# Kernel optimization log

Hardware: AMD Instinct MI355X
Metric: run time of the kernel (lower is better)

## Reference

```python
import jax, jax.numpy as jnp
import numpy as np

OBS_DIM = 512
BACKBONE_DIMS = [1024, 1024, 512]
EXPERT_HIDDEN = 256
NUM_EXPERTS = 16
NUM_ACTIONS = 32
BATCH = 65536


def _glorot(key, shape):
    fan_in = shape[-2] if len(shape) >= 2 else shape[-1]
    return jax.random.normal(key, shape, dtype=jnp.float32) * (1.0 / np.sqrt(fan_in))


def setup_inputs() -> dict:
    key = jax.random.key(0)
    ks = jax.random.split(key, 16)
    inp = {}
    inp['obs'] = jax.random.normal(ks[0], (BATCH, OBS_DIM), dtype=jnp.float32)
    # shared backbone: 512->1024->1024->512 (Linear+ReLU+Dropout(eval=identity))
    dims = [OBS_DIM] + BACKBONE_DIMS
    for i in range(3):
        inp[f'Wb{i}'] = _glorot(ks[1 + i], (dims[i], dims[i + 1]))
        inp[f'bb{i}'] = jnp.zeros((dims[i + 1],), dtype=jnp.float32)
    # experts, batched over expert dim: 512->256->ReLU->256->32
    inp['We1'] = _glorot(ks[4], (NUM_EXPERTS, BACKBONE_DIMS[-1], EXPERT_HIDDEN))
    inp['be1'] = jnp.zeros((NUM_EXPERTS, EXPERT_HIDDEN), dtype=jnp.float32)
    inp['We2'] = _glorot(ks[5], (NUM_EXPERTS, EXPERT_HIDDEN, NUM_ACTIONS))
    inp['be2'] = jnp.zeros((NUM_EXPERTS, NUM_ACTIONS), dtype=jnp.float32)
    # motion selector: 512->256->128->16 + softmax
    inp['Ws0'] = _glorot(ks[6], (OBS_DIM, 256))
    inp['bs0'] = jnp.zeros((256,), dtype=jnp.float32)
    inp['Ws1'] = _glorot(ks[7], (256, 128))
    inp['bs1'] = jnp.zeros((128,), dtype=jnp.float32)
    inp['Ws2'] = _glorot(ks[8], (128, NUM_EXPERTS))
    inp['bs2'] = jnp.zeros((NUM_EXPERTS,), dtype=jnp.float32)
    return inp


def reference(obs, Wb0, bb0, Wb1, bb1, Wb2, bb2, We1, be1, We2, be2,
              Ws0, bs0, Ws1, bs1, Ws2, bs2):
    # shared backbone (Dropout is identity in eval/inference)
    h = jax.nn.relu(obs @ Wb0 + bb0)
    h = jax.nn.relu(h @ Wb1 + bb1)
    h = jax.nn.relu(h @ Wb2 + bb2)  # [B, 512]
    # all experts on shared features, as one batched GEMM
    eh = jax.nn.relu(jnp.einsum('bd,edh->beh', h, We1) + be1)       # [B, E, 256]
    expert_actions = jnp.einsum('beh,eha->bea', eh, We2) + be2       # [B, E, A]
    # motion selector (softmax fusion weights)
    s = jax.nn.relu(obs @ Ws0 + bs0)
    s = jax.nn.relu(s @ Ws1 + bs1)
    w = jax.nn.softmax(s @ Ws2 + bs2, axis=-1)                        # [B, E]
    # softmax-weighted fusion over experts
    fused = jnp.einsum('bea,be->ba', expert_actions, w)              # [B, A]
    return fused
```

## Files before the change

kernel.cpp:

```cpp
#include <hip/hip_runtime.h>
#include <hip/hip_bf16.h>
#include <stdint.h>

typedef __attribute__((ext_vector_type(8))) short short8;
typedef __attribute__((ext_vector_type(4))) float f32x4;

__device__ __forceinline__ float b2f(short s) {
    union { unsigned u; float f; } v; v.u = ((unsigned)(unsigned short)s) << 16; return v.f;
}
__device__ __forceinline__ short f2b(float f) {
    union { float f; unsigned u; } v; v.f = f;
    unsigned r = (v.u + 0x7FFF + ((v.u >> 16) & 1)) >> 16;
    return (short)r;
}

__device__ __forceinline__ void gload16(const void* g, void* l) {
    __builtin_amdgcn_global_load_lds(
        (const __attribute__((address_space(1))) void*)(uintptr_t)g,
        (__attribute__((address_space(3))) void*)(uintptr_t)l,
        16, 0, 0);
}

#define BAR()    asm volatile("s_barrier" ::: "memory")
#define WAITV0() asm volatile("s_waitcnt vmcnt(0)" ::: "memory")
#define WAITL0() asm volatile("s_waitcnt lgkmcnt(0)" ::: "memory")
#define SGB()    __builtin_amdgcn_sched_barrier(0)

__global__ __launch_bounds__(256) void cast_bf16_kernel(
    const float* __restrict__ src, short* __restrict__ dst, int n8) {
    int i = blockIdx.x * 256 + threadIdx.x;
    if (i >= n8) return;
    const float4* s = (const float4*)src + (size_t)i * 2;
    float4 x0 = s[0], x1 = s[1];
    short8 o;
    o[0] = f2b(x0.x); o[1] = f2b(x0.y); o[2] = f2b(x0.z); o[3] = f2b(x0.w);
    o[4] = f2b(x1.x); o[5] = f2b(x1.y); o[6] = f2b(x1.z); o[7] = f2b(x1.w);
    *((short8*)dst + i) = o;
}

__global__ __launch_bounds__(256) void transpose_cast_kernel(
    const float* __restrict__ W, short* __restrict__ Wt, int K, int N, int total) {
    int t = blockIdx.x * 256 + threadIdx.x;
    if (t >= total) return;
    const float* src = W + (size_t)blockIdx.y * K * N;
    short* dst = Wt + (size_t)blockIdx.y * K * N;
    int n = t % N;
    int k0 = (t / N) * 8;
    short8 o;
#pragma unroll
    for (int i = 0; i < 8; i++) o[i] = f2b(src[(size_t)(k0 + i) * N + n]);
    *(short8*)(dst + (size_t)n * K + k0) = o;
}

__global__ __launch_bounds__(256, 3)
void gemm_bt_bias_relu(const short* __restrict__ A, const short* __restrict__ Bt,
                       const float* __restrict__ bias, short* __restrict__ C,
                       int M, int N, int K) {
    __shared__ __align__(16) short As[128 * 32];
    __shared__ __align__(16) short Bs[128 * 32];
    const int tid = threadIdx.x;
    const int w = tid >> 6, lane = tid & 63;
    const int tm = blockIdx.y * 128, tn = blockIdx.x * 128;
    const int wm = (w & 1) * 64, wn = (w >> 1) * 64;
    const int r = lane & 15, q = lane >> 4, qk = q * 8;

    const int c0 = w * 2, c1 = w * 2 + 1;
    const int srow0 = c0 * 16 + (lane >> 2);
    const int srow1 = c1 * 16 + (lane >> 2);
    const int skk = (lane & 3) * 8;
    const short* gA0 = A + (size_t)(tm + srow0) * K + skk;
    const short* gA1 = A + (size_t)(tm + srow1) * K + skk;
    const short* gB0 = Bt + (size_t)(tn + srow0) * K + skk;
    const short* gB1 = Bt + (size_t)(tn + srow1) * K + skk;
    short* lA0 = &As[c0 * 512]; short* lA1 = &As[c1 * 512];
    short* lB0 = &Bs[c0 * 512]; short* lB1 = &Bs[c1 * 512];

    f32x4 acc[4][4] = {};
    for (int k0 = 0; k0 < K; k0 += 32) {
        gload16(gA0 + k0, lA0);
        gload16(gA1 + k0, lA1);
        gload16(gB0 + k0, lB0);
        gload16(gB1 + k0, lB1);
        __syncthreads();
        short8 a[4], b[4];
#pragma unroll
        for (int i = 0; i < 4; i++) a[i] = *(const short8*)&As[(wm + i * 16 + r) * 32 + qk];
#pragma unroll
        for (int j = 0; j < 4; j++) b[j] = *(const short8*)&Bs[(wn + j * 16 + r) * 32 + qk];
#pragma unroll
        for (int i = 0; i < 4; i++)
#pragma unroll
            for (int j = 0; j < 4; j++)
                acc[i][j] = __builtin_amdgcn_mfma_f32_16x16x32_bf16(a[i], b[j], acc[i][j], 0, 0, 0);
        __syncthreads();
    }
#pragma unroll
    for (int j = 0; j < 4; j++) {
        int col = tn + wn + j * 16 + r;
        float bj = bias[col];
#pragma unroll
        for (int i = 0; i < 4; i++)
#pragma unroll
            for (int rr = 0; rr < 4; rr++) {
                int row = tm + wm + i * 16 + q * 4 + rr;
                float v = fmaxf(acc[i][j][rr] + bj, 0.f);
                C[(size_t)row * N + col] = f2b(v);
            }
    }
}

__global__ __launch_bounds__(256)
void selector_softmax(const short* __restrict__ s1, const short* __restrict__ Ws2t,
                      const float* __restrict__ bs2, float* __restrict__ wsel) {
    int tid = threadIdx.x;
    int row = blockIdx.x * 16 + (tid >> 4);
    int e = tid & 15;
    const short8* a = (const short8*)(s1 + (size_t)row * 128);
    const short8* b = (const short8*)(Ws2t + (size_t)e * 128);
    float acc = bs2[e];
#pragma unroll
    for (int kk = 0; kk < 16; ++kk) {
        short8 av = a[kk], bv = b[kk];
#pragma unroll
        for (int i = 0; i < 8; i++) acc = fmaf(b2f(av[i]), b2f(bv[i]), acc);
    }
    float m = acc;
#pragma unroll
    for (int off = 8; off >= 1; off >>= 1) m = fmaxf(m, __shfl_xor(m, off, 16));
    float ex = __expf(acc - m);
    float s = ex;
#pragma unroll
    for (int off = 8; off >= 1; off >>= 1) s += __shfl_xor(s, off, 16);
    wsel[(size_t)row * 16 + e] = ex / s;
}

__global__ __launch_bounds__(256)
void out_init_kernel(const float* __restrict__ wsel, const float* __restrict__ be2,
                     float* __restrict__ out) {
    int i = blockIdx.x * 256 + threadIdx.x;
    int row = i >> 5, a = i & 31;
    const float* wr = wsel + (size_t)row * 16;
    float acc = 0.f;
#pragma unroll
    for (int e = 0; e < 16; e++) acc = fmaf(wr[e], be2[e * 32 + a], acc);
    out[i] = acc;
}

__global__ __launch_bounds__(256)
void reduce_kernel(const float* __restrict__ partial, float* __restrict__ out) {
    int t = blockIdx.x * 256 + threadIdx.x;
    int a4 = t & 7, i = t >> 3;
    int by = i >> 8, r = i & 255;
    const float* p = partial + (size_t)by * 16 * 8192 + r * 32 + a4 * 4;
    f32x4 s = *(const f32x4*)(out + (size_t)i * 32 + a4 * 4);
#pragma unroll
    for (int bx = 0; bx < 16; bx++) s += *(const f32x4*)(p + (size_t)bx * 8192);
    *(f32x4*)(out + (size_t)i * 32 + a4 * 4) = s;
}

template<int MODE>
__global__ __launch_bounds__(512, 2)
void gemm256(const short* __restrict__ A, const short* __restrict__ Bt,
             const float* __restrict__ bias, const float* __restrict__ wselp,
             const short* __restrict__ W2, short* __restrict__ C,
             float* __restrict__ pout, int M, int N, int K) {
    extern __shared__ __align__(16) short lds[];
    const int tid = threadIdx.x;
    const int w = tid >> 6, lane = tid & 63;
    const int wr = w >> 2, wc = w & 3;

    const int gx = gridDim.x;
    const int b = blockIdx.y * gx + blockIdx.x;
    const int per = (gx * gridDim.y) >> 3;
    const int sb = (b & 7) * per + (b >> 3);
    const int bx = sb % gx, by = sb / gx;
    const int tm = by * 256, tn = bx * 256;

    const int rih = w * 8 + (lane >> 3);
    const int colel = (((lane & 7) ^ (lane >> 3)) << 3);
    const short* pA = A + (size_t)(tm + rih) * K + colel;
    const short* pB = Bt + (size_t)(tn + rih) * K + colel;
    const size_t rK64 = (size_t)64 * K, rK128 = (size_t)128 * K;
    short* const ldsw = lds + w * 512;

#define STG_A(buf, h, t) do { \
        const short* s_ = pA + (size_t)(h) * rK128 + (size_t)(t) * 64; \
        short* d_ = ldsw + (buf) * 32768 + (h) * 8192; \
        gload16(s_, d_); \
        gload16(s_ + rK64, d_ + 4096); } while (0)
#define STG_B(buf, h, t) do { \
        const short* s_ = pB + (size_t)(h) * rK128 + (size_t)(t) * 64; \
        short* d_ = ldsw + (buf) * 32768 + 16384 + (h) * 8192; \
        gload16(s_, d_); \
        gload16(s_ + rK64, d_ + 4096); } while (0)

    const int rA = lane & 15, q = lane >> 4;
    const int csw0 = ((q << 4)) ^ ((lane & 7) << 4);
    const int csw1 = (64 + (q << 4)) ^ ((lane & 7) << 4);
    const char* const ldsB_ = (const char*)lds;
    const int aBase0 = wr * 16384 + rA * 128;
    const int bBase0 = 32768 + (wc >> 1) * 16384 + ((wc & 1) * 64 + rA) * 128;

    f32x4 acc[8][4] = {};
    short8 a[4][2], b0[2][2], b1[2][2];
    const int nt = K >> 6;

    STG_A(0, 0, 0); STG_A(0, 1, 0); STG_B(0, 0, 0); STG_B(0, 1, 0);
    WAITV0(); BAR();

    for (int t = 0; t < nt; ++t) {
        const int cur = t & 1, nxt = cur ^ 1;
        const char* pa = ldsB_ + cur * 65536 + aBase0;
        const char* pb = ldsB_ + cur * 65536 + bBase0;
#pragma unroll
        for (int m = 0; m < 4; m++) {
            a[m][0] = *(const short8*)(pa + m * 2048 + csw0);
            a[m][1] = *(const short8*)(pa + m * 2048 + csw1);
        }
#pragma unroll
        for (int n = 0; n < 2; n++) {
            b0[n][0] = *(const short8*)(pb + n * 2048 + csw0);
            b0[n][1] = *(const short8*)(pb + n * 2048 + csw1);
        }
        if (t + 1 < nt) {
            STG_A(nxt, 0, t + 1); STG_A(nxt, 1, t + 1);
            STG_B(nxt, 0, t + 1); STG_B(nxt, 1, t + 1);
        }
        WAITL0(); SGB();
        __builtin_amdgcn_s_setprio(1);
#pragma unroll
        for (int m = 0; m < 4; m++)
#pragma unroll
            for (int n = 0; n < 2; n++) {
                acc[m][n] = __builtin_amdgcn_mfma_f32_16x16x32_bf16(a[m][0], b0[n][0], acc[m][n], 0, 0, 0);
                acc[m][n] = __builtin_amdgcn_mfma_f32_16x16x32_bf16(a[m][1], b0[n][1], acc[m][n], 0, 0, 0);
            }
        __builtin_amdgcn_s_setprio(0);
#pragma unroll
        for (int n = 0; n < 2; n++) {
            b1[n][0] = *(const short8*)(pb + (2 + n) * 2048 + csw0);
            b1[n][1] = *(const short8*)(pb + (2 + n) * 2048 + csw1);
        }
        WAITL0(); SGB();
        __builtin_amdgcn_s_setprio(1);
#pragma unroll
        for (int m = 0; m < 4; m++)
#pragma unroll
            for (int n = 0; n < 2; n++) {
                acc[m][2 + n] = __builtin_amdgcn_mfma_f32_16x16x32_bf16(a[m][0], b1[n][0], acc[m][2 + n], 0, 0, 0);
                acc[m][2 + n] = __builtin_amdgcn_mfma_f32_16x16x32_bf16(a[m][1], b1[n][1], acc[m][2 + n], 0, 0, 0);
            }
        __builtin_amdgcn_s_setprio(0);
#pragma unroll
        for (int m = 0; m < 4; m++) {
            a[m][0] = *(const short8*)(pa + (4 + m) * 2048 + csw0);
            a[m][1] = *(const short8*)(pa + (4 + m) * 2048 + csw1);
        }
        WAITL0(); SGB();
        __builtin_amdgcn_s_setprio(1);
#pragma unroll
        for (int m = 0; m < 4; m++)
#pragma unroll
            for (int n = 0; n < 2; n++) {
                acc[4 + m][2 + n] = __builtin_amdgcn_mfma_f32_16x16x32_bf16(a[m][0], b1[n][0], acc[4 + m][2 + n], 0, 0, 0);
                acc[4 + m][2 + n] = __builtin_amdgcn_mfma_f32_16x16x32_bf16(a[m][1], b1[n][1], acc[4 + m][2 + n], 0, 0, 0);
            }
        __builtin_amdgcn_s_setprio(0);
        __builtin_amdgcn_s_setprio(1);
#pragma unroll
        for (int m = 0; m < 4; m++)
#pragma unroll
            for (int n = 0; n < 2; n++) {
                acc[4 + m][n] = __builtin_amdgcn_mfma_f32_16x16x32_bf16(a[m][0], b0[n][0], acc[4 + m][n], 0, 0, 0);
                acc[4 + m][n] = __builtin_amdgcn_mfma_f32_16x16x32_bf16(a[m][1], b0[n][1], acc[4 + m][n], 0, 0, 0);
            }
        __builtin_amdgcn_s_setprio(0);
        WAITV0();
        BAR();
    }
#undef STG_A
#undef STG_B

    const int q4 = q * 4;
    float biasv[4];
#pragma unroll
    for (int n = 0; n < 4; n++) biasv[n] = bias[tn + wc * 64 + n * 16 + rA];

    if (MODE == 2) {
        const int e = tn >> 8;
        char* ldsc = (char*)lds;
#pragma unroll
        for (int m = 0; m < 8; m++)
#pragma unroll
            for (int rr = 0; rr < 4; rr++) {
                const int row = wr * 128 + m * 16 + q4 + rr;
                const float ws = wselp[(size_t)(tm + row) * 16 + e];
#pragma unroll
                for (int n = 0; n < 4; n++) {
                    const int col = wc * 64 + n * 16 + rA;
                    const float v = fmaxf(acc[m][n][rr] + biasv[n], 0.f) * ws;
                    *(short*)(ldsc + row * 512 + ((col * 2) ^ ((row & 7) << 4))) = f2b(v);
                }
            }
        WAITL0(); BAR();
        f32x4 g2[2][2] = {};
#pragma unroll
        for (int k2 = 0; k2 < 8; ++k2) {
            short8 a2[2], b2[2];
#pragma unroll
            for (int m2 = 0; m2 < 2; m2++) {
                const int row = w * 32 + m2 * 16 + rA;
                a2[m2] = *(const short8*)(ldsc + row * 512 + ((k2 * 64 + q * 16) ^ ((row & 7) << 4)));
            }
#pragma unroll
            for (int n2 = 0; n2 < 2; n2++)
                b2[n2] = *(const short8*)(W2 + (size_t)(e * 32 + n2 * 16 + rA) * 256 + k2 * 32 + q * 8);
#pragma unroll
            for (int m2 = 0; m2 < 2; m2++)
#pragma unroll
                for (int n2 = 0; n2 < 2; n2++)
                    g2[m2][n2] = __builtin_amdgcn_mfma_f32_16x16x32_bf16(a2[m2], b2[n2], g2[m2][n2], 0, 0, 0);
        }
        float* pp = pout + ((size_t)(tm >> 8) * 16 + e) * 8192;
#pragma unroll
        for (int m2 = 0; m2 < 2; m2++)
#pragma unroll
            for (int rr = 0; rr < 4; rr++) {
                const int row = w * 32 + m2 * 16 + q4 + rr;
#pragma unroll
                for (int n2 = 0; n2 < 2; n2++)
                    pp[row * 32 + n2 * 16 + rA] = g2[m2][n2][rr];
            }
        return;
    }

#pragma unroll
    for (int m = 0; m < 8; m++)
#pragma unroll
        for (int rr = 0; rr < 4; rr++) {
            const int row = tm + wr * 128 + m * 16 + q4 + rr;
            float ws = 1.f;
            if (MODE == 1) ws = wselp[(size_t)row * 16 + (tn >> 8)];
#pragma unroll
            for (int n = 0; n < 4; n++) {
                const int col = tn + wc * 64 + n * 16 + rA;
                float v = fmaxf(acc[m][n][rr] + biasv[n], 0.f);
                if (MODE == 1) v *= ws;
                C[(size_t)row * N + col] = f2b(v);
            }
        }
}

extern "C" void kernel_launch(void* const* d_in, const int* in_sizes, int n_in,
                              void* d_out, int out_size, void* d_ws, size_t ws_size,
                              hipStream_t stream) {
    const float* obs = (const float*)d_in[0];
    const float* Wb0 = (const float*)d_in[1]; const float* bb0 = (const float*)d_in[2];
    const float* Wb1 = (const float*)d_in[3]; const float* bb1 = (const float*)d_in[4];
    const float* Wb2 = (const float*)d_in[5]; const float* bb2 = (const float*)d_in[6];
    const float* We1 = (const float*)d_in[7]; const float* be1 = (const float*)d_in[8];
    const float* We2 = (const float*)d_in[9]; const float* be2 = (const float*)d_in[10];
    const float* Ws0 = (const float*)d_in[11]; const float* bs0 = (const float*)d_in[12];
    const float* Ws1 = (const float*)d_in[13]; const float* bs1 = (const float*)d_in[14];
    const float* Ws2 = (const float*)d_in[15]; const float* bs2 = (const float*)d_in[16];

    const int B = 65536;
    char* ws = (char*)d_ws;
    size_t off = 0;
    auto alloc = [&](size_t bytes) { void* p = ws + off; off += (bytes + 255) & ~(size_t)255; return p; };
    short* obs_bf = (short*)alloc((size_t)B * 512 * 2);
    short* h1     = (short*)alloc((size_t)B * 1024 * 2);
    short* h2     = (short*)alloc((size_t)B * 1024 * 2);
    short* hbuf   = (short*)alloc((size_t)B * 512 * 2);
    short* s0     = (short*)alloc((size_t)B * 256 * 2);
    short* s1     = (short*)alloc((size_t)B * 128 * 2);
    float* wsel   = (float*)alloc((size_t)B * 16 * 4);
    short* Wb0t   = (short*)alloc((size_t)512 * 1024 * 2);
    short* Wb1t   = (short*)alloc((size_t)1024 * 1024 * 2);
    short* Wb2t   = (short*)alloc((size_t)1024 * 512 * 2);
    short* We1t   = (short*)alloc((size_t)16 * 512 * 256 * 2);
    short* We2t   = (short*)alloc((size_t)16 * 256 * 32 * 2);
    short* Ws0t   = (short*)alloc((size_t)512 * 256 * 2);
    short* Ws1t   = (short*)alloc((size_t)256 * 128 * 2);
    short* Ws2t   = (short*)alloc((size_t)128 * 16 * 2);
    float* partial = (float*)h1;

    static int inited = 0;
    if (!inited) {
        hipFuncSetAttribute(reinterpret_cast<const void*>(gemm256<0>),
                            hipFuncAttributeMaxDynamicSharedMemorySize, 131072);
        hipFuncSetAttribute(reinterpret_cast<const void*>(gemm256<2>),
                            hipFuncAttributeMaxDynamicSharedMemorySize, 131072);
        inited = 1;
    }

    cast_bf16_kernel<<<(B * 512 / 8 + 255) / 256, 256, 0, stream>>>(obs, obs_bf, B * 512 / 8);
    transpose_cast_kernel<<<dim3((1024 * 512 / 8 + 255) / 256, 1), 256, 0, stream>>>(Wb0, Wb0t, 512, 1024, 1024 * 512 / 8);
    transpose_cast_kernel<<<dim3((1024 * 1024 / 8 + 255) / 256, 1), 256, 0, stream>>>(Wb1, Wb1t, 1024, 1024, 1024 * 1024 / 8);
    transpose_cast_kernel<<<dim3((512 * 1024 / 8 + 255) / 256, 1), 256, 0, stream>>>(Wb2, Wb2t, 1024, 512, 512 * 1024 / 8);
    transpose_cast_kernel<<<dim3((256 * 512 / 8 + 255) / 256, 16), 256, 0, stream>>>(We1, We1t, 512, 256, 256 * 512 / 8);
    transpose_cast_kernel<<<dim3((32 * 256 / 8 + 255) / 256, 16), 256, 0, stream>>>(We2, We2t, 256, 32, 32 * 256 / 8);
    transpose_cast_kernel<<<dim3((256 * 512 / 8 + 255) / 256, 1), 256, 0, stream>>>(Ws0, Ws0t, 512, 256, 256 * 512 / 8);
    transpose_cast_kernel<<<dim3((128 * 256 / 8 + 255) / 256, 1), 256, 0, stream>>>(Ws1, Ws1t, 256, 128, 128 * 256 / 8);
    transpose_cast_kernel<<<dim3((16 * 128 / 8 + 255) / 256, 1), 256, 0, stream>>>(Ws2, Ws2t, 128, 16, 16 * 128 / 8);

    gemm256<0><<<dim3(1, B / 256), 512, 131072, stream>>>(obs_bf, Ws0t, bs0, nullptr, nullptr, s0, nullptr, B, 256, 512);
    gemm_bt_bias_relu<<<dim3(1, B / 128), 256, 0, stream>>>(s0, Ws1t, bs1, s1, B, 128, 256);
    selector_softmax<<<B / 16, 256, 0, stream>>>(s1, Ws2t, bs2, wsel);
    out_init_kernel<<<B * 32 / 256, 256, 0, stream>>>(wsel, be2, (float*)d_out);

    gemm256<0><<<dim3(4, B / 256), 512, 131072, stream>>>(obs_bf, Wb0t, bb0, nullptr, nullptr, h1, nullptr, B, 1024, 512);
    gemm256<0><<<dim3(4, B / 256), 512, 131072, stream>>>(h1, Wb1t, bb1, nullptr, nullptr, h2, nullptr, B, 1024, 1024);
    gemm256<0><<<dim3(2, B / 256), 512, 131072, stream>>>(h2, Wb2t, bb2, nullptr, nullptr, hbuf, nullptr, B, 512, 1024);

    gemm256<2><<<dim3(16, B / 256), 512, 131072, stream>>>(
        hbuf, We1t, be1, wsel, We2t, nullptr, partial, B, 4096, 512);
    reduce_kernel<<<B * 8 / 256, 256, 0, stream>>>(partial, (float*)d_out);
}
```

Measured before the change: 1.033 ms.

## Fuse selector layers, merge obs GEMMs, pipeline LDS fragment loads, remap expert grid

The first selector layer is concatenated with the first backbone layer into one GEMM over obs (N=1280), with a new mode that routes the extra 256 columns to s0. The second selector layer, the final 16-way projection and the softmax are fused into one kernel that keeps s1 in LDS and uses MFMA for the last layer. The main gemm256 loop now prefetches the next tile's A/B fragments after the barrier and drops the explicit lgkmcnt waits and sched barriers, to overlap LDS reads with MFMA. The expert GEMM also gets a different block-to-tile mapping. These cut launches and intermediate traffic, at the cost of more register pressure and a reliance on compiler-inserted waits.

```diff
diff --git a/kernel.cpp b/kernel.cpp
--- a/kernel.cpp
+++ b/kernel.cpp
@@ -23,8 +23,6 @@
 
 #define BAR()    asm volatile("s_barrier" ::: "memory")
 #define WAITV0() asm volatile("s_waitcnt vmcnt(0)" ::: "memory")
-#define WAITL0() asm volatile("s_waitcnt lgkmcnt(0)" ::: "memory")
-#define SGB()    __builtin_amdgcn_sched_barrier(0)
 
 __global__ __launch_bounds__(256) void cast_bf16_kernel(
     const float* __restrict__ src, short* __restrict__ dst, int n8) {
@@ -53,14 +51,15 @@
 }
 
 __global__ __launch_bounds__(256, 3)
-void gemm_bt_bias_relu(const short* __restrict__ A, const short* __restrict__ Bt,
-                       const float* __restrict__ bias, short* __restrict__ C,
-                       int M, int N, int K) {
+void sel_fused(const short* __restrict__ s0, const short* __restrict__ Ws1t,
+               const float* __restrict__ bs1, const short* __restrict__ Ws2t,
+               const float* __restrict__ bs2, float* __restrict__ wsel) {
     __shared__ __align__(16) short As[128 * 32];
     __shared__ __align__(16) short Bs[128 * 32];
+    __shared__ __align__(16) short s1l[128 * 136];
     const int tid = threadIdx.x;
     const int w = tid >> 6, lane = tid & 63;
-    const int tm = blockIdx.y * 128, tn = blockIdx.x * 128;
+    const int tm = blockIdx.x * 128;
     const int wm = (w & 1) * 64, wn = (w >> 1) * 64;
     const int r = lane & 15, q = lane >> 4, qk = q * 8;
 
@@ -68,15 +67,15 @@
     const int srow0 = c0 * 16 + (lane >> 2);
     const int srow1 = c1 * 16 + (lane >> 2);
     const int skk = (lane & 3) * 8;
-    const short* gA0 = A + (size_t)(tm + srow0) * K + skk;
-    const short* gA1 = A + (size_t)(tm + srow1) * K + skk;
-    const short* gB0 = Bt + (size_t)(tn + srow0) * K + skk;
-    const short* gB1 = Bt + (size_t)(tn + srow1) * K + skk;
+    const short* gA0 = s0 + (size_t)(tm + srow0) * 256 + skk;
+    const short* gA1 = s0 + (size_t)(tm + srow1) * 256 + skk;
+    const short* gB0 = Ws1t + (size_t)srow0 * 256 + skk;
+    const short* gB1 = Ws1t + (size_t)srow1 * 256 + skk;
     short* lA0 = &As[c0 * 512]; short* lA1 = &As[c1 * 512];
     short* lB0 = &Bs[c0 * 512]; short* lB1 = &Bs[c1 * 512];
 
     f32x4 acc[4][4] = {};
-    for (int k0 = 0; k0 < K; k0 += 32) {
+    for (int k0 = 0; k0 < 256; k0 += 32) {
         gload16(gA0 + k0, lA0);
         gload16(gA1 + k0, lA1);
         gload16(gB0 + k0, lB0);
@@ -96,42 +95,43 @@
     }
 #pragma unroll
     for (int j = 0; j < 4; j++) {
-        int col = tn + wn + j * 16 + r;
-        float bj = bias[col];
+        int col = wn + j * 16 + r;
+        float bj = bs1[col];
 #pragma unroll
         for (int i = 0; i < 4; i++)
 #pragma unroll
             for (int rr = 0; rr < 4; rr++) {
-                int row = tm + wm + i * 16 + q * 4 + rr;
-                float v = fmaxf(acc[i][j][rr] + bj, 0.f);
-                C[(size_t)row * N + col] = f2b(v);
-            }
-    }
-}
-
-__global__ __launch_bounds__(256)
-void selector_softmax(const short* __restrict__ s1, const short* __restrict__ Ws2t,
-                      const float* __restrict__ bs2, float* __restrict__ wsel) {
-    int tid = threadIdx.x;
-    int row = blockIdx.x * 16 + (tid >> 4);
-    int e = tid & 15;
-    const short8* a = (const short8*)(s1 + (size_t)row * 128);
-    const short8* b = (const short8*)(Ws2t + (size_t)e * 128);
-    float acc = bs2[e];
-#pragma unroll
-    for (int kk = 0; kk < 16; ++kk) {
-        short8 av = a[kk], bv = b[kk];
-#pragma unroll
-        for (int i = 0; i < 8; i++) acc = fmaf(b2f(av[i]), b2f(bv[i]), acc);
-    }
-    float m = acc;
-#pragma unroll
-    for (int off = 8; off >= 1; off >>= 1) m = fmaxf(m, __shfl_xor(m, off, 16));
-    float ex = __expf(acc - m);
-    float s = ex;
-#pragma unroll
-    for (int off = 8; off >= 1; off >>= 1) s += __shfl_xor(s, off, 16);
-    wsel[(size_t)row * 16 + e] = ex / s;
+                int row = wm + i * 16 + q * 4 + rr;
+                s1l[row * 136 + col] = f2b(fmaxf(acc[i][j][rr] + bj, 0.f));
+            }
+    }
+    __syncthreads();
+    f32x4 acc3[2] = {};
+#pragma unroll
+    for (int k3 = 0; k3 < 4; ++k3) {
+        short8 b3 = *(const short8*)(Ws2t + (size_t)r * 128 + k3 * 32 + qk);
+#pragma unroll
+        for (int m2 = 0; m2 < 2; m2++) {
+            short8 a3 = *(const short8*)&s1l[(w * 32 + m2 * 16 + r) * 136 + k3 * 32 + qk];
+            acc3[m2] = __builtin_amdgcn_mfma_f32_16x16x32_bf16(a3, b3, acc3[m2], 0, 0, 0);
+        }
+    }
+    float bse = bs2[r];
+#pragma unroll
+    for (int m2 = 0; m2 < 2; m2++)
+#pragma unroll
+        for (int rr = 0; rr < 4; rr++) {
+            int row = tm + w * 32 + m2 * 16 + q * 4 + rr;
+            float v = acc3[m2][rr] + bse;
+            float m = v;
+#pragma unroll
+            for (int off = 8; off >= 1; off >>= 1) m = fmaxf(m, __shfl_xor(m, off, 16));
+            float ex = __expf(v - m);
+            float s = ex;
+#pragma unroll
+            for (int off = 8; off >= 1; off >>= 1) s += __shfl_xor(s, off, 16);
+            wsel[(size_t)row * 16 + r] = ex / s;
+        }
 }
 
 __global__ __launch_bounds__(256)
@@ -163,7 +163,8 @@
 void gemm256(const short* __restrict__ A, const short* __restrict__ Bt,
              const float* __restrict__ bias, const float* __restrict__ wselp,
              const short* __restrict__ W2, short* __restrict__ C,
-             float* __restrict__ pout, int M, int N, int K) {
+             float* __restrict__ pout, const float* __restrict__ bias2,
+             short* __restrict__ C2, int M, int N, int K) {
     extern __shared__ __align__(16) short lds[];
     const int tid = threadIdx.x;
     const int w = tid >> 6, lane = tid & 63;
@@ -171,9 +172,16 @@
 
     const int gx = gridDim.x;
     const int b = blockIdx.y * gx + blockIdx.x;
-    const int per = (gx * gridDim.y) >> 3;
-    const int sb = (b & 7) * per + (b >> 3);
-    const int bx = sb % gx, by = sb / gx;
+    int bx, by;
+    if (MODE == 2) {
+        const int x = b & 7, i = b >> 3;
+        by = x * 32 + (i >> 4);
+        bx = i & 15;
+    } else {
+        const int per = (gx * gridDim.y) >> 3;
+        const int sb = (b & 7) * per + (b >> 3);
+        bx = sb % gx; by = sb / gx;
+    }
     const int tm = by * 256, tn = bx * 256;
 
     const int rih = w * 8 + (lane >> 3);
@@ -202,68 +210,60 @@
     const int bBase0 = 32768 + (wc >> 1) * 16384 + ((wc & 1) * 64 + rA) * 128;
 
     f32x4 acc[8][4] = {};
-    short8 a[4][2], b0[2][2], b1[2][2];
+    short8 aL[4][2], aH[4][2], b0[2][2], b1[2][2];
     const int nt = K >> 6;
 
     STG_A(0, 0, 0); STG_A(0, 1, 0); STG_B(0, 0, 0); STG_B(0, 1, 0);
     WAITV0(); BAR();
+    {
+        const char* pa = ldsB_ + aBase0;
+        const char* pb = ldsB_ + bBase0;
+#pragma unroll
+        for (int m = 0; m < 4; m++) {
+            aL[m][0] = *(const short8*)(pa + m * 2048 + csw0);
+            aL[m][1] = *(const short8*)(pa + m * 2048 + csw1);
+        }
+#pragma unroll
+        for (int n = 0; n < 2; n++) {
+            b0[n][0] = *(const short8*)(pb + n * 2048 + csw0);
+            b0[n][1] = *(const short8*)(pb + n * 2048 + csw1);
+        }
+    }
 
     for (int t = 0; t < nt; ++t) {
         const int cur = t & 1, nxt = cur ^ 1;
         const char* pa = ldsB_ + cur * 65536 + aBase0;
         const char* pb = ldsB_ + cur * 65536 + bBase0;
 #pragma unroll
-        for (int m = 0; m < 4; m++) {
-            a[m][0] = *(const short8*)(pa + m * 2048 + csw0);
-            a[m][1] = *(const short8*)(pa + m * 2048 + csw1);
-        }
-#pragma unroll
         for (int n = 0; n < 2; n++) {
-            b0[n][0] = *(const short8*)(pb + n * 2048 + csw0);
-            b0[n][1] = *(const short8*)(pb + n * 2048 + csw1);
+            b1[n][0] = *(const short8*)(pb + (2 + n) * 2048 + csw0);
+            b1[n][1] = *(const short8*)(pb + (2 + n) * 2048 + csw1);
         }
         if (t + 1 < nt) {
             STG_A(nxt, 0, t + 1); STG_A(nxt, 1, t + 1);
             STG_B(nxt, 0, t + 1); STG_B(nxt, 1, t + 1);
         }
-        WAITL0(); SGB();
         __builtin_amdgcn_s_setprio(1);
 #pragma unroll
         for (int m = 0; m < 4; m++)
 #pragma unroll
             for (int n = 0; n < 2; n++) {
-                acc[m][n] = __builtin_amdgcn_mfma_f32_16x16x32_bf16(a[m][0], b0[n][0], acc[m][n], 0, 0, 0);
-                acc[m][n] = __builtin_amdgcn_mfma_f32_16x16x32_bf16(a[m][1], b0[n][1], acc[m][n], 0, 0, 0);
+                acc[m][n] = __builtin_amdgcn_mfma_f32_16x16x32_bf16(aL[m][0], b0[n][0], acc[m][n], 0, 0, 0);
+                acc[m][n] = __builtin_amdgcn_mfma_f32_16x16x32_bf16(aL[m][1], b0[n][1], acc[m][n], 0, 0, 0);
             }
         __builtin_amdgcn_s_setprio(0);
 #pragma unroll
-        for (int n = 0; n < 2; n++) {
-            b1[n][0] = *(const short8*)(pb + (2 + n) * 2048 + csw0);
-            b1[n][1] = *(const short8*)(pb + (2 + n) * 2048 + csw1);
-        }
-        WAITL0(); SGB();
+        for (int m = 0; m < 4; m++) {
+            aH[m][0] = *(const short8*)(pa + (4 + m) * 2048 + csw0);
+            aH[m][1] = *(const short8*)(pa + (4 + m) * 2048 + csw1);
+        }
         __builtin_amdgcn_s_setprio(1);
 #pragma unroll
         for (int m = 0; m < 4; m++)
 #pragma unroll
             for (int n = 0; n < 2; n++) {
-                acc[m][2 + n] = __builtin_amdgcn_mfma_f32_16x16x32_bf16(a[m][0], b1[n][0], acc[m][2 + n], 0, 0, 0);
-                acc[m][2 + n] = __builtin_amdgcn_mfma_f32_16x16x32_bf16(a[m][1], b1[n][1], acc[m][2 + n], 0, 0, 0);
-            }
-        __builtin_amdgcn_s_setprio(0);
-#pragma unroll
-        for (int m = 0; m < 4; m++) {
-            a[m][0] = *(const short8*)(pa + (4 + m) * 2048 + csw0);
-            a[m][1] = *(const short8*)(pa + (4 + m) * 2048 + csw1);
-        }
-        WAITL0(); SGB();
-        __builtin_amdgcn_s_setprio(1);
-#pragma unroll
-        for (int m = 0; m < 4; m++)
-#pragma unroll
-            for (int n = 0; n < 2; n++) {
-                acc[4 + m][2 + n] = __builtin_amdgcn_mfma_f32_16x16x32_bf16(a[m][0], b1[n][0], acc[4 + m][2 + n], 0, 0, 0);
-                acc[4 + m][2 + n] = __builtin_amdgcn_mfma_f32_16x16x32_bf16(a[m][1], b1[n][1], acc[4 + m][2 + n], 0, 0, 0);
+                acc[m][2 + n] = __builtin_amdgcn_mfma_f32_16x16x32_bf16(aL[m][0], b1[n][0], acc[m][2 + n], 0, 0, 0);
+                acc[m][2 + n] = __builtin_amdgcn_mfma_f32_16x16x32_bf16(aL[m][1], b1[n][1], acc[m][2 + n], 0, 0, 0);
             }
         __builtin_amdgcn_s_setprio(0);
         __builtin_amdgcn_s_setprio(1);
@@ -271,12 +271,34 @@
         for (int m = 0; m < 4; m++)
 #pragma unroll
             for (int n = 0; n < 2; n++) {
-                acc[4 + m][n] = __builtin_amdgcn_mfma_f32_16x16x32_bf16(a[m][0], b0[n][0], acc[4 + m][n], 0, 0, 0);
-                acc[4 + m][n] = __builtin_amdgcn_mfma_f32_16x16x32_bf16(a[m][1], b0[n][1], acc[4 + m][n], 0, 0, 0);
+                acc[4 + m][2 + n] = __builtin_amdgcn_mfma_f32_16x16x32_bf16(aH[m][0], b1[n][0], acc[4 + m][2 + n], 0, 0, 0);
+                acc[4 + m][2 + n] = __builtin_amdgcn_mfma_f32_16x16x32_bf16(aH[m][1], b1[n][1], acc[4 + m][2 + n], 0, 0, 0);
             }
         __builtin_amdgcn_s_setprio(0);
-        WAITV0();
-        BAR();
+        __builtin_amdgcn_s_setprio(1);
+#pragma unroll
+        for (int m = 0; m < 4; m++)
+#pragma unroll
+            for (int n = 0; n < 2; n++) {
+                acc[4 + m][n] = __builtin_amdgcn_mfma_f32_16x16x32_bf16(aH[m][0], b0[n][0], acc[4 + m][n], 0, 0, 0);
+                acc[4 + m][n] = __builtin_amdgcn_mfma_f32_16x16x32_bf16(aH[m][1], b0[n][1], acc[4 + m][n], 0, 0, 0);
+            }
+        __builtin_amdgcn_s_setprio(0);
+        WAITV0(); BAR();
+        if (t + 1 < nt) {
+            const char* qa = ldsB_ + nxt * 65536 + aBase0;
+            const char* qb = ldsB_ + nxt * 65536 + bBase0;
+#pragma unroll
+            for (int m = 0; m < 4; m++) {
+                aL[m][0] = *(const short8*)(qa + m * 2048 + csw0);
+                aL[m][1] = *(const short8*)(qa + m * 2048 + csw1);
+            }
+#pragma unroll
+            for (int n = 0; n < 2; n++) {
+                b0[n][0] = *(const short8*)(qb + n * 2048 + csw0);
+                b0[n][1] = *(const short8*)(qb + n * 2048 + csw1);
+            }
+        }
     }
 #undef STG_A
 #undef STG_B
@@ -284,7 +306,10 @@
     const int q4 = q * 4;
     float biasv[4];
 #pragma unroll
-    for (int n = 0; n < 4; n++) biasv[n] = bias[tn + wc * 64 + n * 16 + rA];
+    for (int n = 0; n < 4; n++) {
+        const int col = tn + wc * 64 + n * 16 + rA;
+        biasv[n] = (MODE == 3 && tn >= 1024) ? bias2[col - 1024] : bias[col];
+    }
 
     if (MODE == 2) {
         const int e = tn >> 8;
@@ -302,7 +327,8 @@
                     *(short*)(ldsc + row * 512 + ((col * 2) ^ ((row & 7) << 4))) = f2b(v);
                 }
             }
-        WAITL0(); BAR();
+        asm volatile("s_waitcnt lgkmcnt(0)" ::: "memory");
+        BAR();
         f32x4 g2[2][2] = {};
 #pragma unroll
         for (int k2 = 0; k2 < 8; ++k2) {
@@ -339,14 +365,14 @@
 #pragma unroll
         for (int rr = 0; rr < 4; rr++) {
             const int row = tm + wr * 128 + m * 16 + q4 + rr;
-            float ws = 1.f;
-            if (MODE == 1) ws = wselp[(size_t)row * 16 + (tn >> 8)];
 #pragma unroll
             for (int n = 0; n < 4; n++) {
                 const int col = tn + wc * 64 + n * 16 + rA;
                 float v = fmaxf(acc[m][n][rr] + biasv[n], 0.f);
-                if (MODE == 1) v *= ws;
-                C[(size_t)row * N + col] = f2b(v);
+                if (MODE == 3 && tn >= 1024)
+                    C2[(size_t)row * 256 + (col - 1024)] = f2b(v);
+                else
+                    C[(size_t)row * N + col] = f2b(v);
             }
         }
 }
@@ -373,14 +399,12 @@
     short* h2     = (short*)alloc((size_t)B * 1024 * 2);
     short* hbuf   = (short*)alloc((size_t)B * 512 * 2);
     short* s0     = (short*)alloc((size_t)B * 256 * 2);
-    short* s1     = (short*)alloc((size_t)B * 128 * 2);
     float* wsel   = (float*)alloc((size_t)B * 16 * 4);
-    short* Wb0t   = (short*)alloc((size_t)512 * 1024 * 2);
+    short* WbS0t  = (short*)alloc((size_t)1280 * 512 * 2);
     short* Wb1t   = (short*)alloc((size_t)1024 * 1024 * 2);
     short* Wb2t   = (short*)alloc((size_t)1024 * 512 * 2);
     short* We1t   = (short*)alloc((size_t)16 * 512 * 256 * 2);
     short* We2t   = (short*)alloc((size_t)16 * 256 * 32 * 2);
-    short* Ws0t   = (short*)alloc((size_t)512 * 256 * 2);
     short* Ws1t   = (short*)alloc((size_t)256 * 128 * 2);
     short* Ws2t   = (short*)alloc((size_t)128 * 16 * 2);
     float* partial = (float*)h1;
@@ -391,29 +415,32 @@
                             hipFuncAttributeMaxDynamicSharedMemorySize, 131072);
         hipFuncSetAttribute(reinterpret_cast<const void*>(gemm256<2>),
                             hipFuncAttributeMaxDynamicSharedMemorySize, 131072);
+        hipFuncSetAttribute(reinterpret_cast<const void*>(gemm256<3>),
+                            hipFuncAttributeMaxDynamicSharedMemorySize, 131072);
         inited = 1;
     }
 
     cast_bf16_kernel<<<(B * 512 / 8 + 255) / 256, 256, 0, stream>>>(obs, obs_bf, B * 512 / 8);
-    transpose_cast_kernel<<<dim3((1024 * 512 / 8 + 255) / 256, 1), 256, 0, stream>>>(Wb0, Wb0t, 512, 1024, 1024 * 512 / 8);
+    transpose_cast_kernel<<<dim3((1024 * 512 / 8 + 255) / 256, 1), 256, 0, stream>>>(Wb0, WbS0t, 512, 1024, 1024 * 512 / 8);
+    transpose_cast_kernel<<<dim3((256 * 512 / 8 + 255) / 256, 1), 256, 0, stream>>>(Ws0, WbS0t + (size_t)1024 * 512, 512, 256, 256 * 512 / 8);
     transpose_cast_kernel<<<dim3((1024 * 1024 / 8 + 255) / 256, 1), 256, 0, stream>>>(Wb1, Wb1t, 1024, 1024, 1024 * 1024 / 8);
     transpose_cast_kernel<<<dim3((512 * 1024 / 8 + 255) / 256, 1), 256, 0, stream>>>(Wb2, Wb2t, 1024, 512, 512 * 1024 / 8);
     transpose_cast_kernel<<<dim3((256 * 512 / 8 + 255) / 256, 16), 256, 0, stream>>>(We1, We1t, 512, 256, 256 * 512 / 8);
     transpose_cast_kernel<<<dim3((32 * 256 / 8 + 255) / 256, 16), 256, 0, stream>>>(We2, We2t, 256, 32, 32 * 256 / 8);
-    transpose_cast_kernel<<<dim3((256 * 512 / 8 + 255) / 256, 1), 256, 0, stream>>>(Ws0, Ws0t, 512, 256, 256 * 512 / 8);
     transpose_cast_kernel<<<dim3((128 * 256 / 8 + 255) / 256, 1), 256, 0, stream>>>(Ws1, Ws1t, 256, 128, 128 * 256 / 8);
     transpose_cast_kernel<<<dim3((16 * 128 / 8 + 255) / 256, 1), 256, 0, stream>>>(Ws2, Ws2t, 128, 16, 16 * 128 / 8);
 
-    gemm256<0><<<dim3(1, B / 256), 512, 131072, stream>>>(obs_bf, Ws0t, bs0, nullptr, nullptr, s0, nullptr, B, 256, 512);
-    gemm_bt_bias_relu<<<dim3(1, B / 128), 256, 0, stream>>>(s0, Ws1t, bs1, s1, B, 128, 256);
-    selector_softmax<<<B / 16, 256, 0, stream>>>(s1, Ws2t, bs2, wsel);
+    gemm256<3><<<dim3(5, B / 256), 512, 131072, stream>>>(
+        obs_bf, WbS0t, bb0, nullptr, nullptr, h1, nullptr, bs0, s0, B, 1024, 512);
+    sel_fused<<<B / 128, 256, 0, stream>>>(s0, Ws1t, bs1, Ws2t, bs2, wsel);
     out_init_kernel<<<B * 32 / 256, 256, 0, stream>>>(wsel, be2, (float*)d_out);
 
-    gemm256<0><<<dim3(4, B / 256), 512, 131072, stream>>>(obs_bf, Wb0t, bb0, nullptr, nullptr, h1, nullptr, B, 1024, 512);
-    gemm256<0><<<dim3(4, B / 256), 512, 131072, stream>>>(h1, Wb1t, bb1, nullptr, nullptr, h2, nullptr, B, 1024, 1024);
-    gemm256<0><<<dim3(2, B / 256), 512, 131072, stream>>>(h2, Wb2t, bb2, nullptr, nullptr, hbuf, nullptr, B, 512, 1024);
+    gemm256<0><<<dim3(4, B / 256), 512, 131072, stream>>>(
+        h1, Wb1t, bb1, nullptr, nullptr, h2, nullptr, nullptr, nullptr, B, 1024, 1024);
+    gemm256<0><<<dim3(2, B / 256), 512, 131072, stream>>>(
+        h2, Wb2t, bb2, nullptr, nullptr, hbuf, nullptr, nullptr, nullptr, B, 512, 1024);
 
     gemm256<2><<<dim3(16, B / 256), 512, 131072, stream>>>(
-        hbuf, We1t, be1, wsel, We2t, nullptr, partial, B, 4096, 512);
+        hbuf, We1t, be1, wsel, We2t, nullptr, partial, nullptr, nullptr, B, 4096, 512);
     reduce_kernel<<<B * 8 / 256, 256, 0, stream>>>(partial, (float*)d_out);
 }
```

Result: faster. 1.008 ms (-2.4%).
